# Kernel optimization log

Measured on AMD Instinct MI355X. Metric: run time of the kernel, lower is better.

The kernel has to match this reference:

```python
import jax, jax.numpy as jnp
import numpy as np

N_NODES = 100000
N_EDGES = 1600000
IN_CH = 64
HID = 64


def setup_inputs() -> dict:
    key = jax.random.key(0)
    ks = jax.random.split(key, 6)
    x = jax.random.normal(ks[0], (N_NODES, IN_CH), dtype=jnp.float32)
    edge_index = jax.random.randint(ks[1], (2, N_EDGES), 0, N_NODES, dtype=jnp.int64)
    # Glorot-ish scaled weights
    W1 = jax.random.normal(ks[2], (IN_CH, HID), dtype=jnp.float32) / np.sqrt(IN_CH)
    b1 = jnp.zeros((HID,), dtype=jnp.float32)
    W2 = jax.random.normal(ks[3], (HID, HID), dtype=jnp.float32) / np.sqrt(HID)
    b2 = jnp.zeros((HID,), dtype=jnp.float32)
    Wl = jax.random.normal(ks[4], (HID, 1), dtype=jnp.float32) / np.sqrt(HID)
    bl = jnp.zeros((1,), dtype=jnp.float32)
    return {"x": x, "edge_index": edge_index, "W1": W1, "b1": b1,
            "W2": W2, "b2": b2, "Wl": Wl, "bl": bl}


def _gcn_conv(h, W, b, src, dst, norm, n_nodes):
    # GCNConv: linear transform, then sym-normalized neighborhood sum, then bias.
    h = h @ W                                  # [N, out]
    msg = h[src] * norm[:, None]               # [E+N, out] gather + scale
    agg = jax.ops.segment_sum(msg, dst, num_segments=n_nodes)  # scatter-add
    return agg + b


def reference(x, edge_index, W1, b1, W2, b2, Wl, bl):
    n = x.shape[0]
    self_loop = jnp.arange(n, dtype=edge_index.dtype)
    src = jnp.concatenate([edge_index[0], self_loop])  # message sources (x_j)
    dst = jnp.concatenate([edge_index[1], self_loop])  # aggregation targets
    # symmetric normalization deg^{-1/2}[src] * deg^{-1/2}[dst], deg incl. self-loops
    deg = jax.ops.segment_sum(jnp.ones_like(dst, dtype=x.dtype), dst, num_segments=n)
    dinv = jnp.where(deg > 0, jax.lax.rsqrt(jnp.maximum(deg, 1.0)), 0.0)
    norm = dinv[src] * dinv[dst]

    h = jax.nn.relu(_gcn_conv(x, W1, b1, src, dst, norm, n))
    # dropout is identity in eval mode
    h = _gcn_conv(h, W2, b2, src, dst, norm, n)
    return jax.nn.sigmoid(h @ Wl + bl)          # [N, 1]
```

## Files before the change

kernel.cpp:

```cpp
#include <hip/hip_runtime.h>
#include <hip/hip_fp16.h>

#define CH 64
#define NBUCK 1024
#define BSHIFT 7
#define BMASK 127
#define NBLK_P 128

typedef _Float16 f16x4 __attribute__((ext_vector_type(4)));
typedef float    f32x4 __attribute__((ext_vector_type(4)));


__global__ __launch_bounds__(256) void k_hist(const int* __restrict__ dst,
                                              int* __restrict__ blkhist, int E) {
    __shared__ int h[NBUCK];
    for (int i = threadIdx.x; i < NBUCK; i += blockDim.x) h[i] = 0;
    __syncthreads();
    int chunk = (E + NBLK_P - 1) / NBLK_P;
    int beg = blockIdx.x * chunk;
    int end = min(beg + chunk, E);
    for (int e = beg + threadIdx.x; e < end; e += blockDim.x)
        atomicAdd(&h[dst[e] >> BSHIFT], 1);
    __syncthreads();
    for (int i = threadIdx.x; i < NBUCK; i += blockDim.x)
        blkhist[blockIdx.x * NBUCK + i] = h[i];
}

__global__ __launch_bounds__(256) void k_bucketscan(const int* __restrict__ blkhist,
                                                    int* __restrict__ off_t,
                                                    int* __restrict__ tot) {
    int lane = threadIdx.x & 63;
    int t = (blockIdx.x * blockDim.x + threadIdx.x) >> 6;
    int b0 = lane * 2, b1 = b0 + 1;
    int v0 = blkhist[b0 * NBUCK + t];
    int v1 = blkhist[b1 * NBUCK + t];
    int ps = v0 + v1;
    int sc = ps;
#pragma unroll
    for (int o = 1; o < 64; o <<= 1) {
        int u = __shfl_up(sc, o, 64);
        if (lane >= o) sc += u;
    }
    int excl = sc - ps;
    off_t[t * NBLK_P + b0] = excl;
    off_t[t * NBLK_P + b1] = excl + v0;
    if (lane == 63) tot[t] = sc;
}

__global__ __launch_bounds__(1024) void k_scantot(const int* __restrict__ tot,
                                                  int* __restrict__ bbase) {
    __shared__ int sh[NBUCK];
    int t = threadIdx.x;
    int v = tot[t];
    sh[t] = v;
    __syncthreads();
    for (int o = 1; o < NBUCK; o <<= 1) {
        int u = (t >= o) ? sh[t - o] : 0;
        __syncthreads();
        sh[t] += u;
        __syncthreads();
    }
    bbase[t] = sh[t] - v;
    if (t == NBUCK - 1) bbase[NBUCK] = sh[t];
}

__global__ __launch_bounds__(256) void k_partition(const int* __restrict__ src,
                                                   const int* __restrict__ dst,
                                                   const int* __restrict__ off_t,
                                                   const int* __restrict__ bbase,
                                                   unsigned int* __restrict__ ebuf, int E) {
    __shared__ int cur[NBUCK];
    for (int i = threadIdx.x; i < NBUCK; i += blockDim.x)
        cur[i] = bbase[i] + off_t[i * NBLK_P + blockIdx.x];
    __syncthreads();
    int chunk = (E + NBLK_P - 1) / NBLK_P;
    int beg = blockIdx.x * chunk;
    int end = min(beg + chunk, E);
    for (int e = beg + threadIdx.x; e < end; e += blockDim.x) {
        int s = src[e];
        int d = dst[e];
        int p = atomicAdd(&cur[d >> BSHIFT], 1);
        ebuf[p] = ((unsigned int)(d & BMASK) << 17) | (unsigned int)s;
    }
}

__global__ __launch_bounds__(128) void k_bucket_csr(const unsigned int* __restrict__ ebuf,
                                                    const int* __restrict__ bbase,
                                                    int* __restrict__ row_ptr,
                                                    float* __restrict__ dinv,
                                                    int* __restrict__ col, int n) {
    __shared__ int cnt[128];
    __shared__ int cur[128];
    __shared__ int sc[128];
    int t = threadIdx.x;
    int k = blockIdx.x;
    int e0 = bbase[k], e1 = bbase[k + 1];
    cnt[t] = 0;
    __syncthreads();
    for (int e = e0 + t; e < e1; e += 128)
        atomicAdd(&cnt[ebuf[e] >> 17], 1);
    __syncthreads();
    int c = cnt[t];
    int pl = (c + 16) & ~15;
    if (pl < 32) pl = 32;
    sc[t] = pl;
    __syncthreads();
    for (int o = 1; o < 128; o <<= 1) {
        int v = (t >= o) ? sc[t - o] : 0;
        __syncthreads();
        sc[t] += v;
        __syncthreads();
    }
    int prow = e0 + (k << 12) + sc[t] - pl;
    int node = (k << BSHIFT) + t;
    if (node < n) {
        row_ptr[node] = prow | ((pl >> 4) << 24);
        dinv[node] = rsqrtf((float)(c + 1));
    }
    col[prow] = (node < n) ? node : n;
    for (int q = c + 1; q < pl; ++q) col[prow + q] = n;
    cur[t] = prow + 1;
    __syncthreads();
    for (int e = e0 + t; e < e1; e += 128) {
        unsigned int u = ebuf[e];
        int p = atomicAdd(&cur[u >> 17], 1);
        col[p] = (int)(u & 0x1FFFFu);
    }
}


__global__ __launch_bounds__(64) void k_fold(const float* __restrict__ W2,
                                             const float* __restrict__ Wl,
                                             float* __restrict__ wt) {
    int k = threadIdx.x;
    float s = 0.0f;
#pragma unroll 8
    for (int c = 0; c < CH; ++c) s = fmaf(W2[k * CH + c], Wl[c], s);
    wt[k] = s;
}


__global__ __launch_bounds__(256) void k_prep(const float* __restrict__ W,
                                              __half* __restrict__ wfrag) {
    for (int idx = threadIdx.x; idx < 1024; idx += 256) {
        int f = idx >> 6;
        int l = idx & 63;
        int w4 = f >> 2, t = f & 3;
        int kb = w4 * 16 + 4 * (l >> 4);
        int c  = t * 16 + (l & 15);
#pragma unroll
        for (int b = 0; b < 4; ++b) {
            float wv = W[(kb + b) * CH + c];
            __half hi = __float2half(wv);
            float lo = wv - __half2float(hi);
            wfrag[(size_t)f * 256 + l * 4 + b] = hi;
            wfrag[4096 + (size_t)f * 256 + l * 4 + b] = __float2half(lo);
        }
    }
}


__global__ __launch_bounds__(256) void k_gemm_mfma(const float* __restrict__ in,
                                                   const __half* __restrict__ wfrag,
                                                   const float* __restrict__ dinv,
                                                   __half* __restrict__ hs, int n) {
    if (blockIdx.x == 0 && threadIdx.x < CH)
        hs[(size_t)n * CH + threadIdx.x] = __float2half(0.0f);

    int lane = threadIdx.x & 63;
    int wid  = (blockIdx.x * blockDim.x + threadIdx.x) >> 6;
    int nw   = (gridDim.x * blockDim.x) >> 6;

    const f16x4* wf = (const f16x4*)wfrag;
    f16x4 wh[16], wl[16];
#pragma unroll
    for (int f = 0; f < 16; ++f) {
        wh[f] = wf[f * 64 + lane];
        wl[f] = wf[1024 + f * 64 + lane];
    }

    int r15 = lane & 15;
    int q   = lane >> 4;
    int ngrp = (n + 15) >> 4;

    for (int g = wid; g < ngrp; g += nw) {
        int base = g << 4;
        int arow = min(base + r15, n - 1);
        const float* ap = in + (size_t)arow * CH + 4 * q;

        f32x4 acc0 = {0.f, 0.f, 0.f, 0.f};
        f32x4 acc1 = {0.f, 0.f, 0.f, 0.f};
        f32x4 acc2 = {0.f, 0.f, 0.f, 0.f};
        f32x4 acc3 = {0.f, 0.f, 0.f, 0.f};

#pragma unroll
        for (int w4 = 0; w4 < 4; ++w4) {
            float4 xv = *(const float4*)(ap + w4 * 16);
            f16x4 ah, al;
            ah[0] = (_Float16)xv.x; al[0] = (_Float16)(xv.x - (float)ah[0]);
            ah[1] = (_Float16)xv.y; al[1] = (_Float16)(xv.y - (float)ah[1]);
            ah[2] = (_Float16)xv.z; al[2] = (_Float16)(xv.z - (float)ah[2]);
            ah[3] = (_Float16)xv.w; al[3] = (_Float16)(xv.w - (float)ah[3]);

            acc0 = __builtin_amdgcn_mfma_f32_16x16x16f16(ah, wh[w4 * 4 + 0], acc0, 0, 0, 0);
            acc1 = __builtin_amdgcn_mfma_f32_16x16x16f16(ah, wh[w4 * 4 + 1], acc1, 0, 0, 0);
            acc2 = __builtin_amdgcn_mfma_f32_16x16x16f16(ah, wh[w4 * 4 + 2], acc2, 0, 0, 0);
            acc3 = __builtin_amdgcn_mfma_f32_16x16x16f16(ah, wh[w4 * 4 + 3], acc3, 0, 0, 0);
            acc0 = __builtin_amdgcn_mfma_f32_16x16x16f16(al, wh[w4 * 4 + 0], acc0, 0, 0, 0);
            acc1 = __builtin_amdgcn_mfma_f32_16x16x16f16(al, wh[w4 * 4 + 1], acc1, 0, 0, 0);
            acc2 = __builtin_amdgcn_mfma_f32_16x16x16f16(al, wh[w4 * 4 + 2], acc2, 0, 0, 0);
            acc3 = __builtin_amdgcn_mfma_f32_16x16x16f16(al, wh[w4 * 4 + 3], acc3, 0, 0, 0);
            acc0 = __builtin_amdgcn_mfma_f32_16x16x16f16(ah, wl[w4 * 4 + 0], acc0, 0, 0, 0);
            acc1 = __builtin_amdgcn_mfma_f32_16x16x16f16(ah, wl[w4 * 4 + 1], acc1, 0, 0, 0);
            acc2 = __builtin_amdgcn_mfma_f32_16x16x16f16(ah, wl[w4 * 4 + 2], acc2, 0, 0, 0);
            acc3 = __builtin_amdgcn_mfma_f32_16x16x16f16(ah, wl[w4 * 4 + 3], acc3, 0, 0, 0);
        }

#pragma unroll
        for (int b = 0; b < 4; ++b) {
            int row = base + 4 * q + b;
            if (row < n) {
                float d = dinv[row];
                size_t o = (size_t)row * CH + r15;
                hs[o +  0] = __float2half(acc0[b] * d);
                hs[o + 16] = __float2half(acc1[b] * d);
                hs[o + 32] = __float2half(acc2[b] * d);
                hs[o + 48] = __float2half(acc3[b] * d);
            }
        }
    }
}


__global__ __launch_bounds__(256) void k_gather_gemm(const int* __restrict__ row_ptr,
                                                     const int* __restrict__ col,
                                                     const __half2* __restrict__ hs2,
                                                     const float* __restrict__ dinv,
                                                     const float* __restrict__ wt,
                                                     const float* __restrict__ bias,
                                                     float* __restrict__ z, int n) {
    if (blockIdx.x == 0 && threadIdx.x == 0) z[n] = 0.0f;
    int lane = threadIdx.x & 63;
    int l    = lane & 31;
    int g    = lane >> 5;
    int wid  = (blockIdx.x * blockDim.x + threadIdx.x) >> 6;
    int nw   = (gridDim.x * blockDim.x) >> 6;

    float2 wt2 = ((const float2*)wt)[l];
    float2 bi2 = ((const float2*)bias)[l];

    int npairs = (n + 1) >> 1;
    int pr = wid;
    if (pr >= npairs) return;

    unsigned pkA = (unsigned)row_ptr[pr << 1];
    unsigned pkB = (unsigned)row_ptr[min((pr << 1) + 1, n - 1)];
    int cv = col[(g ? (int)(pkB & 0xFFFFFFu) : (int)(pkA & 0xFFFFFFu)) + l];

    for (; pr < npairs; pr += nw) {
        int a = pr << 1;
        bool hasB = (a + 1) < n;
        int begA = (int)(pkA & 0xFFFFFFu), nbA = (int)(pkA >> 24);
        int begB = (int)(pkB & 0xFFFFFFu), nbB = (int)(pkB >> 24);
        int mycv = cv;
        float dA = dinv[a];
        float dB = dinv[hasB ? a + 1 : a];

        __half2 h[32];
#pragma unroll
        for (int r = 0; r < 32; ++r) {
            int idx = __shfl(mycv, r, 32);
            h[r] = hs2[(size_t)idx * 32 + l];
        }

        int nxt = pr + nw;
        if (nxt < npairs) {
            int a1 = nxt << 1;
            pkA = (unsigned)row_ptr[a1];
            pkB = (unsigned)row_ptr[min(a1 + 1, n - 1)];
            cv = col[(g ? (int)(pkB & 0xFFFFFFu) : (int)(pkA & 0xFFFFFFu)) + l];
        }

        float ax0 = 0.f, ay0 = 0.f, ax1 = 0.f, ay1 = 0.f;
        float ax2 = 0.f, ay2 = 0.f, ax3 = 0.f, ay3 = 0.f;
#pragma unroll
        for (int r = 0; r < 32; r += 4) {
            float2 f0 = __half22float2(h[r]);
            float2 f1 = __half22float2(h[r + 1]);
            float2 f2 = __half22float2(h[r + 2]);
            float2 f3 = __half22float2(h[r + 3]);
            ax0 += f0.x; ay0 += f0.y;
            ax1 += f1.x; ay1 += f1.y;
            ax2 += f2.x; ay2 += f2.y;
            ax3 += f3.x; ay3 += f3.y;
        }
        float accx = (ax0 + ax1) + (ax2 + ax3);
        float accy = (ay0 + ay1) + (ay2 + ay3);

        int nbM = max(nbA, nbB);
        if (nbM > 2) {
            int pl = (g ? nbB : nbA) << 4;
            int bg = g ? begB : begA;
            for (int r = 32; r < pl; ++r) {
                float2 f = __half22float2(hs2[(size_t)col[bg + r] * 32 + l]);
                accx += f.x; accy += f.y;
            }
        }

        float d = g ? dB : dA;
        float vx = fmaxf(fmaf(accx, d, bi2.x), 0.0f);
        float vy = fmaxf(fmaf(accy, d, bi2.y), 0.0f);
        float p = fmaf(vx, wt2.x, vy * wt2.y);
#pragma unroll
        for (int o = 16; o > 0; o >>= 1) p += __shfl_xor(p, o, 64);
        p *= d;
        if (l == 0 && (g == 0 || hasB)) z[a + g] = p;
    }
}


__global__ __launch_bounds__(256) void k_head(const int* __restrict__ row_ptr,
                                              const int* __restrict__ col,
                                              const float* __restrict__ z,
                                              const float* __restrict__ dinv,
                                              const float* __restrict__ b2,
                                              const float* __restrict__ Wl,
                                              const float* __restrict__ bl,
                                              float* __restrict__ out, int n) {
    int lane = threadIdx.x & 63;
    float c0 = b2[lane] * Wl[lane];
#pragma unroll
    for (int o = 32; o > 0; o >>= 1) c0 += __shfl_xor(c0, o, 64);
    c0 += bl[0];

    int tid = blockIdx.x * blockDim.x + threadIdx.x;
    int st  = gridDim.x * blockDim.x;
    for (int node = tid; node < n; node += st) {
        unsigned pk = (unsigned)row_ptr[node];
        int beg = (int)(pk & 0xFFFFFFu);
        int m   = (int)(pk >> 24) << 4;
        float s = 0.0f;
        for (int e = 0; e < m; e += 4) {
            float t0 = z[col[beg + e]];
            float t1 = z[col[beg + e + 1]];
            float t2 = z[col[beg + e + 2]];
            float t3 = z[col[beg + e + 3]];
            s += t0; s += t1; s += t2; s += t3;
        }
        float v = dinv[node] * s + c0;
        out[node] = 1.0f / (1.0f + expf(-v));
    }
}


extern "C" void kernel_launch(void* const* d_in, const int* in_sizes, int n_in,
                              void* d_out, int out_size, void* d_ws, size_t ws_size,
                              hipStream_t stream) {
    const float* x   = (const float*)d_in[0];
    const int*   ei  = (const int*)d_in[1];
    const float* W1  = (const float*)d_in[2];
    const float* b1  = (const float*)d_in[3];
    const float* W2  = (const float*)d_in[4];
    const float* b2  = (const float*)d_in[5];
    const float* Wl  = (const float*)d_in[6];
    const float* bl  = (const float*)d_in[7];
    float*       out = (float*)d_out;

    const int N = in_sizes[0] / CH;
    const int E = in_sizes[1] / 2;
    const int* src = ei;
    const int* dst = ei + E;

    const size_t Npad = ((size_t)N + 511) & ~(size_t)511;
    const size_t Epad = ((size_t)E + 511) & ~(size_t)511;
    const size_t COLSZ = Epad + (size_t)NBUCK * 4096 + 512;

    float* z        = (float*)d_ws;
    float* dinv     = z + Npad;
    int*   row_ptr  = (int*)(dinv + Npad);
    float* wt       = (float*)(row_ptr + Npad);
    __half* wfrag   = (__half*)(wt + 512);
    int*   col      = (int*)(wfrag + 8192);
    unsigned int* ebuf = (unsigned int*)(col + COLSZ);
    int*   blkhist  = (int*)(ebuf + Epad);
    int*   off_t    = blkhist + NBLK_P * NBUCK;
    int*   bbase    = off_t + NBLK_P * NBUCK;
    int*   tot      = bbase + NBUCK + 64;
    __half* A       = (__half*)ebuf;

    const int TB = 256;
    const int GRID = 2048;
    const int NB_USED = (N + BMASK) >> BSHIFT;

    k_fold<<<1, 64, 0, stream>>>(W2, Wl, wt);
    k_prep<<<1, 256, 0, stream>>>(W1, wfrag);

    k_hist<<<NBLK_P, TB, 0, stream>>>(dst, blkhist, E);
    k_bucketscan<<<NBUCK * 64 / TB, TB, 0, stream>>>(blkhist, off_t, tot);
    k_scantot<<<1, NBUCK, 0, stream>>>(tot, bbase);
    k_partition<<<NBLK_P, TB, 0, stream>>>(src, dst, off_t, bbase, ebuf, E);
    k_bucket_csr<<<NB_USED, 128, 0, stream>>>(ebuf, bbase, row_ptr, dinv, col, N);

    k_gemm_mfma<<<784, TB, 0, stream>>>(x, wfrag, dinv, A, N);

    k_gather_gemm<<<2 * GRID, TB, 0, stream>>>(row_ptr, col, (const __half2*)A, dinv,
                                               wt, b1, z, N);

    k_head<<<(N + TB - 1) / TB, TB, 0, stream>>>(row_ptr, col, z, dinv, b2, Wl, bl, out, N);
}
```

Measured before the change: 214.9 us.

## Drop padded CSR rows, handle self-loop separately, widen partition grid, merge init kernels

CSR rows are now stored compactly with the exact degree packed into row_ptr, replacing the 16-aligned padding and the in-row self-loop entry. The gather and head kernels add the self term explicitly and mask unused slots to the zero row, which removes the padding writes and the extra column reads. The partition/histogram grid goes from 128 to 512 blocks, with the bucket scan handling 8 values per lane. The two small weight-prep kernels are merged into one launch. The gather still issues 32 loads per node regardless of degree, now pointing masked slots at the zero row, and depends on hs row n being zero.

```diff
diff --git a/kernel.cpp b/kernel.cpp
--- a/kernel.cpp
+++ b/kernel.cpp
@@ -5,7 +5,8 @@
 #define NBUCK 1024
 #define BSHIFT 7
 #define BMASK 127
-#define NBLK_P 128
+#define NBLK_P 512
+#define RPMASK 0x1FFFFFu
 
 typedef _Float16 f16x4 __attribute__((ext_vector_type(4)));
 typedef float    f32x4 __attribute__((ext_vector_type(4)));
@@ -31,19 +32,24 @@
                                                     int* __restrict__ tot) {
     int lane = threadIdx.x & 63;
     int t = (blockIdx.x * blockDim.x + threadIdx.x) >> 6;
-    int b0 = lane * 2, b1 = b0 + 1;
-    int v0 = blkhist[b0 * NBUCK + t];
-    int v1 = blkhist[b1 * NBUCK + t];
-    int ps = v0 + v1;
-    int sc = ps;
+    int v[8], pre[8];
+    int sum = 0;
+#pragma unroll
+    for (int j = 0; j < 8; ++j) {
+        v[j] = blkhist[(lane * 8 + j) * NBUCK + t];
+        pre[j] = sum;
+        sum += v[j];
+    }
+    int sc = sum;
 #pragma unroll
     for (int o = 1; o < 64; o <<= 1) {
         int u = __shfl_up(sc, o, 64);
         if (lane >= o) sc += u;
     }
-    int excl = sc - ps;
-    off_t[t * NBLK_P + b0] = excl;
-    off_t[t * NBLK_P + b1] = excl + v0;
+    int excl = sc - sum;
+#pragma unroll
+    for (int j = 0; j < 8; ++j)
+        off_t[t * NBLK_P + lane * 8 + j] = excl + pre[j];
     if (lane == 63) tot[t] = sc;
 }
 
@@ -101,9 +107,7 @@
         atomicAdd(&cnt[ebuf[e] >> 17], 1);
     __syncthreads();
     int c = cnt[t];
-    int pl = (c + 16) & ~15;
-    if (pl < 32) pl = 32;
-    sc[t] = pl;
+    sc[t] = c;
     __syncthreads();
     for (int o = 1; o < 128; o <<= 1) {
         int v = (t >= o) ? sc[t - o] : 0;
@@ -111,15 +115,14 @@
         sc[t] += v;
         __syncthreads();
     }
-    int prow = e0 + (k << 12) + sc[t] - pl;
+    int excl = sc[t] - c;
+    int prow = e0 + excl;
     int node = (k << BSHIFT) + t;
     if (node < n) {
-        row_ptr[node] = prow | ((pl >> 4) << 24);
+        row_ptr[node] = prow | (c << 21);
         dinv[node] = rsqrtf((float)(c + 1));
     }
-    col[prow] = (node < n) ? node : n;
-    for (int q = c + 1; q < pl; ++q) col[prow + q] = n;
-    cur[t] = prow + 1;
+    cur[t] = prow;
     __syncthreads();
     for (int e = e0 + t; e < e1; e += 128) {
         unsigned int u = ebuf[e];
@@ -129,19 +132,18 @@
 }
 
 
-__global__ __launch_bounds__(64) void k_fold(const float* __restrict__ W2,
-                                             const float* __restrict__ Wl,
-                                             float* __restrict__ wt) {
-    int k = threadIdx.x;
-    float s = 0.0f;
+__global__ __launch_bounds__(256) void k_init(const float* __restrict__ W2,
+                                              const float* __restrict__ Wl,
+                                              float* __restrict__ wt,
+                                              const float* __restrict__ W1,
+                                              __half* __restrict__ wfrag) {
+    if (threadIdx.x < 64) {
+        int k = threadIdx.x;
+        float s = 0.0f;
 #pragma unroll 8
-    for (int c = 0; c < CH; ++c) s = fmaf(W2[k * CH + c], Wl[c], s);
-    wt[k] = s;
-}
-
-
-__global__ __launch_bounds__(256) void k_prep(const float* __restrict__ W,
-                                              __half* __restrict__ wfrag) {
+        for (int c = 0; c < CH; ++c) s = fmaf(W2[k * CH + c], Wl[c], s);
+        wt[k] = s;
+    }
     for (int idx = threadIdx.x; idx < 1024; idx += 256) {
         int f = idx >> 6;
         int l = idx & 63;
@@ -150,7 +152,7 @@
         int c  = t * 16 + (l & 15);
 #pragma unroll
         for (int b = 0; b < 4; ++b) {
-            float wv = W[(kb + b) * CH + c];
+            float wv = W1[(kb + b) * CH + c];
             __half hi = __float2half(wv);
             float lo = wv - __half2float(hi);
             wfrag[(size_t)f * 256 + l * 4 + b] = hi;
@@ -239,7 +241,6 @@
                                                      const float* __restrict__ wt,
                                                      const float* __restrict__ bias,
                                                      float* __restrict__ z, int n) {
-    if (blockIdx.x == 0 && threadIdx.x == 0) z[n] = 0.0f;
     int lane = threadIdx.x & 63;
     int l    = lane & 31;
     int g    = lane >> 5;
@@ -255,13 +256,15 @@
 
     unsigned pkA = (unsigned)row_ptr[pr << 1];
     unsigned pkB = (unsigned)row_ptr[min((pr << 1) + 1, n - 1)];
-    int cv = col[(g ? (int)(pkB & 0xFFFFFFu) : (int)(pkA & 0xFFFFFFu)) + l];
+    int cv = col[(int)((g ? pkB : pkA) & RPMASK) + l];
 
     for (; pr < npairs; pr += nw) {
         int a = pr << 1;
         bool hasB = (a + 1) < n;
-        int begA = (int)(pkA & 0xFFFFFFu), nbA = (int)(pkA >> 24);
-        int begB = (int)(pkB & 0xFFFFFFu), nbB = (int)(pkB >> 24);
+        int begS = (int)((g ? pkB : pkA) & RPMASK);
+        int degS = (int)((g ? pkB : pkA) >> 21);
+        int degA = (int)(pkA >> 21), degB = (int)(pkB >> 21);
+        int selfS = g ? (hasB ? a + 1 : a) : a;
         int mycv = cv;
         float dA = dinv[a];
         float dB = dinv[hasB ? a + 1 : a];
@@ -269,20 +272,26 @@
         __half2 h[32];
 #pragma unroll
         for (int r = 0; r < 32; ++r) {
-            int idx = __shfl(mycv, r, 32);
+            int cr = __shfl(mycv, r, 32);
+            int idx = (r < degS) ? cr : n;
             h[r] = hs2[(size_t)idx * 32 + l];
         }
+        __half2 hself = hs2[(size_t)selfS * 32 + l];
 
         int nxt = pr + nw;
         if (nxt < npairs) {
             int a1 = nxt << 1;
             pkA = (unsigned)row_ptr[a1];
             pkB = (unsigned)row_ptr[min(a1 + 1, n - 1)];
-            cv = col[(g ? (int)(pkB & 0xFFFFFFu) : (int)(pkA & 0xFFFFFFu)) + l];
-        }
-
-        float ax0 = 0.f, ay0 = 0.f, ax1 = 0.f, ay1 = 0.f;
+            cv = col[(int)((g ? pkB : pkA) & RPMASK) + l];
+        }
+
+        float ax0, ay0, ax1 = 0.f, ay1 = 0.f;
         float ax2 = 0.f, ay2 = 0.f, ax3 = 0.f, ay3 = 0.f;
+        {
+            float2 fs = __half22float2(hself);
+            ax0 = fs.x; ay0 = fs.y;
+        }
 #pragma unroll
         for (int r = 0; r < 32; r += 4) {
             float2 f0 = __half22float2(h[r]);
@@ -297,12 +306,9 @@
         float accx = (ax0 + ax1) + (ax2 + ax3);
         float accy = (ay0 + ay1) + (ay2 + ay3);
 
-        int nbM = max(nbA, nbB);
-        if (nbM > 2) {
-            int pl = (g ? nbB : nbA) << 4;
-            int bg = g ? begB : begA;
-            for (int r = 32; r < pl; ++r) {
-                float2 f = __half22float2(hs2[(size_t)col[bg + r] * 32 + l]);
+        if (max(degA, degB) > 32) {
+            for (int r = 32; r < degS; ++r) {
+                float2 f = __half22float2(hs2[(size_t)col[begS + r] * 32 + l]);
                 accx += f.x; accy += f.y;
             }
         }
@@ -337,16 +343,18 @@
     int st  = gridDim.x * blockDim.x;
     for (int node = tid; node < n; node += st) {
         unsigned pk = (unsigned)row_ptr[node];
-        int beg = (int)(pk & 0xFFFFFFu);
-        int m   = (int)(pk >> 24) << 4;
-        float s = 0.0f;
-        for (int e = 0; e < m; e += 4) {
+        int beg = (int)(pk & RPMASK);
+        int deg = (int)(pk >> 21);
+        float s = z[node];
+        int e = 0;
+        for (; e + 4 <= deg; e += 4) {
             float t0 = z[col[beg + e]];
             float t1 = z[col[beg + e + 1]];
             float t2 = z[col[beg + e + 2]];
             float t3 = z[col[beg + e + 3]];
             s += t0; s += t1; s += t2; s += t3;
         }
+        for (; e < deg; ++e) s += z[col[beg + e]];
         float v = dinv[node] * s + c0;
         out[node] = 1.0f / (1.0f + expf(-v));
     }
@@ -373,7 +381,7 @@
 
     const size_t Npad = ((size_t)N + 511) & ~(size_t)511;
     const size_t Epad = ((size_t)E + 511) & ~(size_t)511;
-    const size_t COLSZ = Epad + (size_t)NBUCK * 4096 + 512;
+    const size_t COLSZ = Epad + 512;
 
     float* z        = (float*)d_ws;
     float* dinv     = z + Npad;
@@ -383,8 +391,8 @@
     int*   col      = (int*)(wfrag + 8192);
     unsigned int* ebuf = (unsigned int*)(col + COLSZ);
     int*   blkhist  = (int*)(ebuf + Epad);
-    int*   off_t    = blkhist + NBLK_P * NBUCK;
-    int*   bbase    = off_t + NBLK_P * NBUCK;
+    int*   off_t    = blkhist + (size_t)NBLK_P * NBUCK;
+    int*   bbase    = off_t + (size_t)NBLK_P * NBUCK;
     int*   tot      = bbase + NBUCK + 64;
     __half* A       = (__half*)ebuf;
 
@@ -392,8 +400,7 @@
     const int GRID = 2048;
     const int NB_USED = (N + BMASK) >> BSHIFT;
 
-    k_fold<<<1, 64, 0, stream>>>(W2, Wl, wt);
-    k_prep<<<1, 256, 0, stream>>>(W1, wfrag);
+    k_init<<<1, TB, 0, stream>>>(W2, Wl, wt, W1, wfrag);
 
     k_hist<<<NBLK_P, TB, 0, stream>>>(dst, blkhist, E);
     k_bucketscan<<<NBUCK * 64 / TB, TB, 0, stream>>>(blkhist, off_t, tot);
```

After: 196.5 us. -8.5%, faster.
